# Kernel tuning notes

Measured on AMD Instinct MI355X. Metric: run time of the kernel, lower is better.

Reference implementation:

```python
import jax, jax.numpy as jnp
import numpy as np

N_LAYER, N_HEAD, D_MODEL, D_K, D_HIDDEN = 8, 8, 512, 64, 2048
N_CONTEXT, N_DICT, MAG = 1024, 8192, 0.05
B, T = 8, 1024


def _sinusoidal_pos(n_context, d_model):
    i2 = np.arange(0, d_model, 2)
    inv = 1.0 / (10000.0 ** (i2 / d_model))
    ang = np.arange(n_context, dtype=np.float32)[:, None] * inv[None, :]
    pe = np.zeros((1, n_context, d_model), np.float32)
    pe[0, :, 0::2] = np.sin(ang)
    pe[0, :, 1::2] = np.cos(ang)
    return jnp.asarray(pe)


def setup_inputs() -> dict:
    key = jax.random.key(0)
    ks = jax.random.split(key, 10)
    p = lambda k, *s: jax.random.normal(k, s, jnp.float32) * MAG
    return {
        "x": jax.random.randint(ks[0], (B, T), 0, N_DICT),
        "last_only": False,
        "capture_stats": False,
        "embedding": p(ks[1], N_DICT, D_MODEL),
        "pos_embedding": _sinusoidal_pos(N_CONTEXT, D_MODEL),  # fixedpos='True', not trained
        "wq": p(ks[2], N_LAYER, N_HEAD, D_MODEL, D_K),
        "wk": p(ks[3], N_LAYER, N_HEAD, D_MODEL, D_K),
        "wv": p(ks[4], N_LAYER, N_HEAD, D_MODEL, D_MODEL),
        "mlp0": p(ks[5], N_LAYER, D_MODEL, D_HIDDEN),
        "mlpb": p(ks[6], N_LAYER, 1, D_HIDDEN),
        "mlp1": p(ks[7], N_LAYER, D_HIDDEN, D_MODEL),
        "unembedding": p(ks[8], D_MODEL, N_DICT),
        "bias": p(ks[9], 1, 1, N_DICT),
    }


def _ln(x):
    # torch LayerNorm(elementwise_affine=False, bias=False), eps=1e-5, biased var
    mu = jnp.mean(x, axis=-1, keepdims=True)
    var = jnp.mean((x - mu) ** 2, axis=-1, keepdims=True)
    return (x - mu) * jax.lax.rsqrt(var + 1e-5)


def reference(x, last_only, capture_stats, embedding, pos_embedding,
              wq, wk, wv, mlp0, mlpb, mlp1, unembedding, bias):
    del capture_stats  # stats path disabled (capture_stats=False)
    t = x.shape[1]
    h = embedding[x] + pos_embedding[:, :t, :]   # [B,T,M]
    h = _ln(h)                                    # enorm='True', lmul = 1/ldiv = 1
    mask = jnp.tril(jnp.ones((t, t), dtype=bool))

    def layer(h, params):
        wq_l, wk_l, wv_l, m0, mb, m1 = params
        q = jnp.einsum('btm,hmq->bhtq', h, wq_l)
        k = jnp.einsum('bom,hmk->bhok', h, wk_l)
        v = jnp.einsum('bom,hmv->bhov', h, wv_l)
        attn = jnp.einsum('bhtq,bhoq->bhto', q, k)
        # exp(clamp(.,max=50)) then tril then sum-normalize (NOT softmax)
        attn = jnp.where(mask, jnp.exp(jnp.minimum(attn, 50.0)), 0.0)
        attn = attn / (jnp.sum(attn, axis=-1, keepdims=True) + 1e-10)
        vsum = jnp.einsum('bhto,bhov->btv', attn, v)  # sums over heads
        h = _ln(h + vsum)                              # amul = 1, lmul = 1
        y = jax.nn.relu(jnp.einsum('btm,mh->bth', h, m0) + mb)
        y = jnp.einsum('bth,hm->btm', y, m1)
        h = _ln(h + y)                                 # pmul = 1, lmul = 1
        return h, None

    h, _ = jax.lax.scan(layer, h, (wq, wk, wv, mlp0, mlpb, mlp1))
    if last_only:
        h = h[:, -1:, :]
    return jnp.einsum('btm,md->btd', h, unembedding) + bias
```

## Files before the change

kernel.cpp:

```cpp
#include <hip/hip_runtime.h>
#include <hip/hip_bf16.h>

#define BB 8
#define TT 1024
#define DM 512
#define NH 8
#define DK 64
#define DH 2048
#define NL 8
#define ND 8192

typedef __attribute__((ext_vector_type(8))) short short8v;
typedef __attribute__((ext_vector_type(8))) _Float16 f16x8;
typedef __attribute__((ext_vector_type(4))) float f32x4;
typedef __attribute__((ext_vector_type(4))) unsigned short ushort4v;
typedef unsigned short u16;

#define MFMA16(a, b, c) __builtin_amdgcn_mfma_f32_16x16x32_bf16(a, b, c, 0, 0, 0)
#define MFMAH(a, b, c)  __builtin_amdgcn_mfma_f32_16x16x32_f16(a, b, c, 0, 0, 0)

__device__ __forceinline__ u16 bf16_bits(float f) {
  union { __hip_bfloat16 h; u16 u; } cv;
  cv.h = __float2bfloat16(f);
  return cv.u;
}
__device__ __forceinline__ float bits_to_f32(u16 u) {
  union { __hip_bfloat16 h; u16 u; } cv;
  cv.u = u;
  return __bfloat162float(cv.h);
}

__device__ __forceinline__ void gload16(const void* g, void* l) {
  __builtin_amdgcn_global_load_lds(
      (const __attribute__((address_space(1))) unsigned int*)g,
      (__attribute__((address_space(3))) unsigned int*)l, 16, 0, 0);
}

#define WAITVM(N) asm volatile("s_waitcnt vmcnt(" #N ")" ::: "memory")
#define WAITLGKM() asm volatile("s_waitcnt lgkmcnt(0)" ::: "memory")
#define BAR() { __builtin_amdgcn_s_barrier(); asm volatile("" ::: "memory"); }

__device__ __forceinline__ void block_reduce2(float& a, float& b) {
  #pragma unroll
  for (int off = 32; off > 0; off >>= 1) {
    a += __shfl_down(a, off, 64);
    b += __shfl_down(b, off, 64);
  }
  __shared__ float sa[4], sb[4];
  int w = threadIdx.x >> 6;
  if ((threadIdx.x & 63) == 0) { sa[w] = a; sb[w] = b; }
  __syncthreads();
  if (threadIdx.x == 0) {
    sa[0] = sa[0] + sa[1] + sa[2] + sa[3];
    sb[0] = sb[0] + sb[1] + sb[2] + sb[3];
  }
  __syncthreads();
  a = sa[0]; b = sb[0];
}

__global__ __launch_bounds__(256) void embed_ln_kernel(
    const int* __restrict__ x, const float* __restrict__ emb,
    const float* __restrict__ pos, float* __restrict__ h,
    u16* __restrict__ hh, _Float16* __restrict__ hf) {
  int bt = blockIdx.x;
  int t = bt & (TT - 1);
  int tid = threadIdx.x;
  int row = x[bt];
  float v0 = emb[(size_t)row * DM + tid]       + pos[(size_t)t * DM + tid];
  float v1 = emb[(size_t)row * DM + tid + 256] + pos[(size_t)t * DM + tid + 256];
  float s = v0 + v1, sq = v0 * v0 + v1 * v1;
  block_reduce2(s, sq);
  float mu  = s * (1.0f / DM);
  float var = sq * (1.0f / DM) - mu * mu;
  float rs  = rsqrtf(var + 1e-5f);
  float r0 = (v0 - mu) * rs, r1 = (v1 - mu) * rs;
  h[(size_t)bt * DM + tid] = r0;
  h[(size_t)bt * DM + tid + 256] = r1;
  hh[(size_t)bt * DM + tid] = bf16_bits(r0);
  hh[(size_t)bt * DM + tid + 256] = bf16_bits(r1);
  hf[(size_t)bt * DM + tid] = (_Float16)r0;
  hf[(size_t)bt * DM + tid + 256] = (_Float16)r1;
}

template<bool BF16ADD>
__global__ __launch_bounds__(256) void ln_residual_kernel(
    float* __restrict__ h, const void* __restrict__ add_,
    u16* __restrict__ hh, _Float16* __restrict__ hf) {
  int bt = blockIdx.x;
  int tid = threadIdx.x;
  float v0 = h[(size_t)bt * DM + tid];
  float v1 = h[(size_t)bt * DM + tid + 256];
  if (BF16ADD) {
    const u16* add = (const u16*)add_;
    v0 += bits_to_f32(add[(size_t)bt * DM + tid]);
    v1 += bits_to_f32(add[(size_t)bt * DM + tid + 256]);
  } else {
    const float* add = (const float*)add_;
    v0 += add[(size_t)bt * DM + tid];
    v1 += add[(size_t)bt * DM + tid + 256];
  }
  float s = v0 + v1, sq = v0 * v0 + v1 * v1;
  block_reduce2(s, sq);
  float mu  = s * (1.0f / DM);
  float var = sq * (1.0f / DM) - mu * mu;
  float rs  = rsqrtf(var + 1e-5f);
  float r0 = (v0 - mu) * rs, r1 = (v1 - mu) * rs;
  h[(size_t)bt * DM + tid] = r0;
  h[(size_t)bt * DM + tid + 256] = r1;
  hh[(size_t)bt * DM + tid] = bf16_bits(r0);
  hh[(size_t)bt * DM + tid + 256] = bf16_bits(r1);
  hf[(size_t)bt * DM + tid] = (_Float16)r0;
  hf[(size_t)bt * DM + tid + 256] = (_Float16)r1;
}

__global__ __launch_bounds__(256) void transpose_hT(
    const float* __restrict__ h, u16* __restrict__ hT) {
  __shared__ float T[64][65];
  int t0 = blockIdx.x * 64;
  int d0 = blockIdx.y * 64;
  int tid = threadIdx.x;
  #pragma unroll
  for (int rep = 0; rep < 16; ++rep) {
    int idx = rep * 256 + tid;
    int i = idx >> 6, j = idx & 63;
    T[i][j] = h[(size_t)(t0 + i) * DM + d0 + j];
  }
  __syncthreads();
  #pragma unroll
  for (int rep = 0; rep < 16; ++rep) {
    int idx = rep * 256 + tid;
    int j = idx >> 6, i = idx & 63;
    hT[(size_t)(d0 + j) * (BB * TT) + t0 + i] = bf16_bits(T[i][j]);
  }
}

__global__ __launch_bounds__(256) void transpose_layer(
    const float* __restrict__ wq, const float* __restrict__ wk,
    const float* __restrict__ wv, const float* __restrict__ w0,
    const float* __restrict__ w1,
    _Float16* __restrict__ qkT, u16* __restrict__ vT2,
    u16* __restrict__ t0o, u16* __restrict__ t1o) {
  __shared__ float T[64][65];
  int t = blockIdx.x;
  const float* in;
  _Float16* of = nullptr;
  u16* ob = nullptr;
  int K, Nb;
  bool vmode = false;
  if (t < 64)       { in = wq; of = qkT;          K = 512;  Nb = 64; }
  else if (t < 128) { in = wk; of = qkT + 262144; K = 512;  Nb = 64;   t -= 64; }
  else if (t < 640) { in = wv; ob = vT2;          K = 512;  Nb = 512;  t -= 128; vmode = true; }
  else if (t < 896) { in = w0; ob = t0o;          K = 512;  Nb = 2048; t -= 640; }
  else              { in = w1; ob = t1o;          K = 2048; Nb = 512;  t -= 896; }
  int ntx = K >> 6;
  int k0 = (t % ntx) * 64, n0 = (t / ntx) * 64;
  int g = n0 / Nb;
  const float* src = in + (size_t)g * K * Nb + (n0 - g * Nb);
  int tid = threadIdx.x;
  #pragma unroll
  for (int rep = 0; rep < 16; ++rep) {
    int idx = rep * 256 + tid;
    int i = idx >> 6, j = idx & 63;
    T[i][j] = src[(size_t)(k0 + i) * Nb + j];
  }
  __syncthreads();
  #pragma unroll
  for (int rep = 0; rep < 16; ++rep) {
    int idx = rep * 256 + tid;
    int j = idx >> 6, i = idx & 63;
    float v = T[i][j];
    if (vmode) {
      vT2[(size_t)(n0 - g * Nb + j) * (NH * DM) + g * Nb + k0 + i] = bf16_bits(v);
    } else if (of) {
      of[(size_t)(n0 + j) * K + k0 + i] = (_Float16)v;
    } else {
      ob[(size_t)(n0 + j) * K + k0 + i] = bf16_bits(v);
    }
  }
}

__global__ __launch_bounds__(256) void transpose_ue(
    const float* __restrict__ ue, u16* __restrict__ ueT) {
  __shared__ float T[64][65];
  int tid = threadIdx.x;
  int k0 = blockIdx.x * 64, n0 = blockIdx.y * 64;
  #pragma unroll
  for (int rep = 0; rep < 16; ++rep) {
    int idx = rep * 256 + tid;
    int i = idx >> 6, j = idx & 63;
    T[i][j] = ue[(size_t)(k0 + i) * ND + n0 + j];
  }
  __syncthreads();
  #pragma unroll
  for (int rep = 0; rep < 16; ++rep) {
    int idx = rep * 256 + tid;
    int j = idx >> 6, i = idx & 63;
    ueT[(size_t)(n0 + j) * DM + k0 + i] = bf16_bits(T[i][j]);
  }
}

template<int MODE>
__global__ __launch_bounds__(256, 2) void gemm_mfma(
    const u16* __restrict__ A, const u16* __restrict__ Bt,
    const float* __restrict__ bias, void* __restrict__ Oo,
    int M, int N, int K) {
  __shared__ u16 As[2][8192];
  __shared__ u16 Bs[2][8192];
  int tid = threadIdx.x;
  int lane = tid & 63, w = tid >> 6;
  int l15 = lane & 15, g = lane >> 4;
  int m0 = blockIdx.x * 128, n0 = blockIdx.y * 128;
  int wr = w >> 1, wc = w & 1;
  int nt = K >> 6;

  f32x4 acc[4][4];
  #pragma unroll
  for (int i = 0; i < 4; ++i)
    #pragma unroll
    for (int j = 0; j < 4; ++j)
      #pragma unroll
      for (int r = 0; r < 4; ++r) acc[i][j][r] = 0.f;

  auto stage = [&](int t, int buf) {
    int k0 = t << 6;
    #pragma unroll
    for (int j = 0; j < 4; ++j) {
      int idx = j * 256 + tid;
      int row = idx >> 3, cs = (idx & 7) ^ (row & 7);
      gload16(A + (size_t)(m0 + row) * K + k0 + cs * 8, &As[buf][idx * 8]);
    }
    #pragma unroll
    for (int j = 0; j < 4; ++j) {
      int idx = j * 256 + tid;
      int row = idx >> 3, cs = (idx & 7) ^ (row & 7);
      gload16(Bt + (size_t)(n0 + row) * K + k0 + cs * 8, &Bs[buf][idx * 8]);
    }
  };

  stage(0, 0);
  for (int t = 0; t < nt; ++t) {
    int cur = t & 1;
    if (t + 1 < nt) {
      stage(t + 1, cur ^ 1);
      WAITVM(8);
    } else {
      WAITVM(0);
    }
    BAR();
    short8v af[4][2], bf[4][2];
    #pragma unroll
    for (int mi = 0; mi < 4; ++mi) {
      int row = wr * 64 + mi * 16 + l15;
      #pragma unroll
      for (int ks = 0; ks < 2; ++ks) {
        int ch = (ks * 4 + g) ^ (row & 7);
        af[mi][ks] = *(const short8v*)&As[cur][row * 64 + ch * 8];
      }
    }
    #pragma unroll
    for (int ni = 0; ni < 4; ++ni) {
      int row = wc * 64 + ni * 16 + l15;
      #pragma unroll
      for (int ks = 0; ks < 2; ++ks) {
        int ch = (ks * 4 + g) ^ (row & 7);
        bf[ni][ks] = *(const short8v*)&Bs[cur][row * 64 + ch * 8];
      }
    }
    __builtin_amdgcn_s_setprio(1);
    #pragma unroll
    for (int mi = 0; mi < 4; ++mi)
      #pragma unroll
      for (int ni = 0; ni < 4; ++ni) {
        acc[mi][ni] = MFMA16(af[mi][0], bf[ni][0], acc[mi][ni]);
        acc[mi][ni] = MFMA16(af[mi][1], bf[ni][1], acc[mi][ni]);
      }
    __builtin_amdgcn_s_setprio(0);
    BAR();
  }

  #pragma unroll
  for (int mi = 0; mi < 4; ++mi) {
    #pragma unroll
    for (int ni = 0; ni < 4; ++ni) {
      int mrow = m0 + wr * 64 + mi * 16 + g * 4;
      int ncol = n0 + wc * 64 + ni * 16 + l15;
      if (MODE == 1) {
        float bv = bias[ncol];
        #pragma unroll
        for (int r = 0; r < 4; ++r)
          ((u16*)Oo)[(size_t)(mrow + r) * N + ncol] =
              bf16_bits(fmaxf(acc[mi][ni][r] + bv, 0.f));
      } else if (MODE == 2) {
        #pragma unroll
        for (int r = 0; r < 4; ++r)
          ((float*)Oo)[(size_t)(mrow + r) * N + ncol] = acc[mi][ni][r];
      } else if (MODE == 3) {
        float bv = bias[ncol];
        #pragma unroll
        for (int r = 0; r < 4; ++r)
          ((float*)Oo)[(size_t)(mrow + r) * N + ncol] = acc[mi][ni][r] + bv;
      } else {
        #pragma unroll
        for (int r = 0; r < 4; ++r)
          ((u16*)Oo)[(size_t)(mrow + r) * N + ncol] = bf16_bits(acc[mi][ni][r]);
      }
    }
  }
}

template<int MODE>
__global__ __launch_bounds__(256, 2) void gemm_n64(
    const u16* __restrict__ A, const u16* __restrict__ Bt,
    void* __restrict__ Oo, int M, int N, int K) {
  __shared__ u16 As[2][8192];
  __shared__ u16 Bs[2][4096];
  int tid = threadIdx.x;
  int lane = tid & 63, w = tid >> 6;
  int l15 = lane & 15, g = lane >> 4;
  int m0 = blockIdx.x * 128, n0 = blockIdx.y * 64;
  int wr = w >> 1, wc = w & 1;
  int nt = K >> 6;

  f32x4 acc[4][2];
  #pragma unroll
  for (int i = 0; i < 4; ++i)
    #pragma unroll
    for (int j = 0; j < 2; ++j)
      #pragma unroll
      for (int r = 0; r < 4; ++r) acc[i][j][r] = 0.f;

  auto stage = [&](int t, int buf) {
    int k0 = t << 6;
    #pragma unroll
    for (int j = 0; j < 4; ++j) {
      int idx = j * 256 + tid;
      int row = idx >> 3, cs = (idx & 7) ^ (row & 7);
      gload16(A + (size_t)(m0 + row) * K + k0 + cs * 8, &As[buf][idx * 8]);
    }
    #pragma unroll
    for (int j = 0; j < 2; ++j) {
      int idx = j * 256 + tid;
      int row = idx >> 3, cs = (idx & 7) ^ (row & 7);
      gload16(Bt + (size_t)(n0 + row) * K + k0 + cs * 8, &Bs[buf][idx * 8]);
    }
  };

  stage(0, 0);
  for (int t = 0; t < nt; ++t) {
    int cur = t & 1;
    if (t + 1 < nt) {
      stage(t + 1, cur ^ 1);
      WAITVM(6);
    } else {
      WAITVM(0);
    }
    BAR();
    short8v af[4][2], bf[2][2];
    #pragma unroll
    for (int mi = 0; mi < 4; ++mi) {
      int row = wr * 64 + mi * 16 + l15;
      #pragma unroll
      for (int ks = 0; ks < 2; ++ks) {
        int ch = (ks * 4 + g) ^ (row & 7);
        af[mi][ks] = *(const short8v*)&As[cur][row * 64 + ch * 8];
      }
    }
    #pragma unroll
    for (int ni = 0; ni < 2; ++ni) {
      int row = wc * 32 + ni * 16 + l15;
      #pragma unroll
      for (int ks = 0; ks < 2; ++ks) {
        int ch = (ks * 4 + g) ^ (row & 7);
        bf[ni][ks] = *(const short8v*)&Bs[cur][row * 64 + ch * 8];
      }
    }
    __builtin_amdgcn_s_setprio(1);
    #pragma unroll
    for (int mi = 0; mi < 4; ++mi)
      #pragma unroll
      for (int ni = 0; ni < 2; ++ni) {
        acc[mi][ni] = MFMA16(af[mi][0], bf[ni][0], acc[mi][ni]);
        acc[mi][ni] = MFMA16(af[mi][1], bf[ni][1], acc[mi][ni]);
      }
    __builtin_amdgcn_s_setprio(0);
    BAR();
  }

  #pragma unroll
  for (int mi = 0; mi < 4; ++mi) {
    #pragma unroll
    for (int ni = 0; ni < 2; ++ni) {
      int mrow = m0 + wr * 64 + mi * 16 + g * 4;
      int ncol = n0 + wc * 32 + ni * 16 + l15;
      if (MODE == 2) {
        #pragma unroll
        for (int r = 0; r < 4; ++r)
          ((float*)Oo)[(size_t)(mrow + r) * N + ncol] = acc[mi][ni][r];
      } else {
        #pragma unroll
        for (int r = 0; r < 4; ++r)
          ((u16*)Oo)[(size_t)(mrow + r) * N + ncol] = bf16_bits(acc[mi][ni][r]);
      }
    }
  }
}

__global__ __launch_bounds__(256, 2) void gemm_qk_f16(
    const _Float16* __restrict__ A, const _Float16* __restrict__ Bt,
    _Float16* __restrict__ Oq, int K) {
  __shared__ _Float16 As[2][8192];
  __shared__ _Float16 Bs[2][8192];
  int tid = threadIdx.x;
  int lane = tid & 63, w = tid >> 6;
  int l15 = lane & 15, g = lane >> 4;
  int m0 = blockIdx.x * 128, n0 = blockIdx.y * 128;
  int wr = w >> 1, wc = w & 1;
  int nt = K >> 6;

  f32x4 acc[4][4];
  #pragma unroll
  for (int i = 0; i < 4; ++i)
    #pragma unroll
    for (int j = 0; j < 4; ++j)
      #pragma unroll
      for (int r = 0; r < 4; ++r) acc[i][j][r] = 0.f;

  auto stage = [&](int t, int buf) {
    int k0 = t << 6;
    #pragma unroll
    for (int j = 0; j < 4; ++j) {
      int idx = j * 256 + tid;
      int row = idx >> 3, cs = (idx & 7) ^ (row & 7);
      gload16(A + (size_t)(m0 + row) * K + k0 + cs * 8, &As[buf][idx * 8]);
    }
    #pragma unroll
    for (int j = 0; j < 4; ++j) {
      int idx = j * 256 + tid;
      int row = idx >> 3, cs = (idx & 7) ^ (row & 7);
      gload16(Bt + (size_t)(n0 + row) * K + k0 + cs * 8, &Bs[buf][idx * 8]);
    }
  };

  stage(0, 0);
  for (int t = 0; t < nt; ++t) {
    int cur = t & 1;
    if (t + 1 < nt) {
      stage(t + 1, cur ^ 1);
      WAITVM(8);
    } else {
      WAITVM(0);
    }
    BAR();
    f16x8 af[4][2], bf[4][2];
    #pragma unroll
    for (int mi = 0; mi < 4; ++mi) {
      int row = wr * 64 + mi * 16 + l15;
      #pragma unroll
      for (int ks = 0; ks < 2; ++ks) {
        int ch = (ks * 4 + g) ^ (row & 7);
        af[mi][ks] = *(const f16x8*)&As[cur][row * 64 + ch * 8];
      }
    }
    #pragma unroll
    for (int ni = 0; ni < 4; ++ni) {
      int row = wc * 64 + ni * 16 + l15;
      #pragma unroll
      for (int ks = 0; ks < 2; ++ks) {
        int ch = (ks * 4 + g) ^ (row & 7);
        bf[ni][ks] = *(const f16x8*)&Bs[cur][row * 64 + ch * 8];
      }
    }
    __builtin_amdgcn_s_setprio(1);
    #pragma unroll
    for (int mi = 0; mi < 4; ++mi)
      #pragma unroll
      for (int ni = 0; ni < 4; ++ni) {
        acc[mi][ni] = MFMAH(af[mi][0], bf[ni][0], acc[mi][ni]);
        acc[mi][ni] = MFMAH(af[mi][1], bf[ni][1], acc[mi][ni]);
      }
    __builtin_amdgcn_s_setprio(0);
    BAR();
  }

  #pragma unroll
  for (int mi = 0; mi < 4; ++mi) {
    #pragma unroll
    for (int ni = 0; ni < 4; ++ni) {
      int mrow = m0 + wr * 64 + mi * 16 + g * 4;
      int ncol = n0 + wc * 64 + ni * 16 + l15;
      _Float16* dst = Oq;
      int nc = ncol;
      if (nc >= 512) { dst = Oq + 4194304; nc -= 512; }
      int head = nc >> 6, dk = nc & (DK - 1);
      int bb = mrow >> 10;
      #pragma unroll
      for (int r = 0; r < 4; ++r) {
        int t = (mrow + r) & (TT - 1);
        dst[(((size_t)bb * NH + head) * TT + t) * DK + dk] = (_Float16)acc[mi][ni][r];
      }
    }
  }
}

__global__ __launch_bounds__(256, 2) void attn_mfma_kernel(
    const _Float16* __restrict__ qp, const _Float16* __restrict__ kp,
    const u16* __restrict__ hT, u16* __restrict__ o) {
  __shared__ __align__(16) u16 Pl[2][64 * 64];
  __shared__ __align__(16) _Float16 Kl[2][64 * 64];
  __shared__ float rs_lds[64];

  int tid = threadIdx.x;
  int lane = tid & 63;
  int w = tid >> 6;
  int l15 = lane & 15, g = lane >> 4;
  int blk = blockIdx.x;
  int bh = blk & 63;
  int tt = 15 - (blk >> 6);
  int b = bh >> 3;

  if (tid < 64) rs_lds[tid] = 0.f;

  auto stageK = [&](int ot, int buf) {
    int ob = ot * 64;
    #pragma unroll
    for (int j = 0; j < 2; ++j) {
      int idx = j * 256 + tid;
      int row = idx >> 3, cs = (idx & 7) ^ (row & 7);
      gload16(kp + ((size_t)bh * TT + ob + row) * DK + cs * 8, &Kl[buf][idx * 8]);
    }
  };

  size_t qbase = (((size_t)bh * TT) + tt * 64 + w * 16 + l15) * DK + g * 8;
  f16x8 qf[2];
  qf[0] = *(const f16x8*)(qp + qbase);
  qf[1] = *(const f16x8*)(qp + qbase + 32);

  f32x4 oacc[4][8];
  #pragma unroll
  for (int qt = 0; qt < 4; ++qt)
    #pragma unroll
    for (int dv = 0; dv < 8; ++dv)
      #pragma unroll
      for (int r = 0; r < 4; ++r) oacc[qt][dv][r] = 0.f;

  stageK(0, 0);
  WAITVM(0);
  __syncthreads();

  for (int ot = 0; ot <= tt; ++ot) {
    int ob = ot * 64;
    bool diag = (ot == tt);
    int buf = ot & 1;
    if (ot < tt) stageK(ot + 1, buf ^ 1);
    f32x4 sacc[4];
    #pragma unroll
    for (int ct = 0; ct < 4; ++ct)
      #pragma unroll
      for (int r = 0; r < 4; ++r) sacc[ct][r] = 0.f;
    __builtin_amdgcn_s_setprio(1);
    #pragma unroll
    for (int ct = 0; ct < 4; ++ct) {
      int row = ct * 16 + l15;
      f16x8 k0 = *(const f16x8*)&Kl[buf][row * 64 + ((g) ^ (row & 7)) * 8];
      f16x8 k1 = *(const f16x8*)&Kl[buf][row * 64 + ((4 + g) ^ (row & 7)) * 8];
      sacc[ct] = MFMAH(qf[0], k0, sacc[ct]);
      sacc[ct] = MFMAH(qf[1], k1, sacc[ct]);
    }
    __builtin_amdgcn_s_setprio(0);
    size_t vbase = ((size_t)(w * 128 + l15)) * (BB * TT) + b * TT + ob + g * 8;
    short8v vf0[8];
    #pragma unroll
    for (int dv = 0; dv < 8; ++dv)
      vf0[dv] = *(const short8v*)(hT + vbase + (size_t)dv * 16 * (BB * TT));
    float psum[4] = {0.f, 0.f, 0.f, 0.f};
    #pragma unroll
    for (int ct = 0; ct < 4; ++ct) {
      #pragma unroll
      for (int r = 0; r < 4; ++r) {
        float s = sacc[ct][r];
        float p = __expf(fminf(s, 50.f));
        if (diag && (ct * 16 + l15 > w * 16 + g * 4 + r)) p = 0.f;
        psum[r] += p;
        int q = w * 16 + g * 4 + r;
        int byte = (q * 128 + (ct * 16 + l15) * 2) ^ ((q & 7) << 4);
        *(u16*)((char*)Pl[buf] + byte) = bf16_bits(p);
      }
    }
    #pragma unroll
    for (int r = 0; r < 4; ++r) {
      float v = psum[r];
      v += __shfl_xor(v, 1, 16);
      v += __shfl_xor(v, 2, 16);
      v += __shfl_xor(v, 4, 16);
      v += __shfl_xor(v, 8, 16);
      if (l15 == 0) rs_lds[w * 16 + g * 4 + r] += v;
    }
    WAITVM(8);
    WAITLGKM();
    BAR();
    short8v vf1[8];
    #pragma unroll
    for (int dv = 0; dv < 8; ++dv)
      vf1[dv] = *(const short8v*)(hT + vbase + 32 + (size_t)dv * 16 * (BB * TT));
    short8v pf[4];
    #pragma unroll
    for (int qt = 0; qt < 4; ++qt) {
      int q = qt * 16 + l15;
      int byte = (q * 128 + g * 16) ^ ((q & 7) << 4);
      pf[qt] = *(short8v*)((char*)Pl[buf] + byte);
    }
    __builtin_amdgcn_s_setprio(1);
    #pragma unroll
    for (int dv = 0; dv < 8; ++dv)
      #pragma unroll
      for (int qt = 0; qt < 4; ++qt)
        oacc[qt][dv] = MFMA16(pf[qt], vf0[dv], oacc[qt][dv]);
    __builtin_amdgcn_s_setprio(0);
    #pragma unroll
    for (int qt = 0; qt < 4; ++qt) {
      int q = qt * 16 + l15;
      int byte = (q * 128 + 64 + g * 16) ^ ((q & 7) << 4);
      pf[qt] = *(short8v*)((char*)Pl[buf] + byte);
    }
    __builtin_amdgcn_s_setprio(1);
    #pragma unroll
    for (int dv = 0; dv < 8; ++dv)
      #pragma unroll
      for (int qt = 0; qt < 4; ++qt)
        oacc[qt][dv] = MFMA16(pf[qt], vf1[dv], oacc[qt][dv]);
    __builtin_amdgcn_s_setprio(0);
  }
  __syncthreads();
  int hh2 = bh & 7;
  #pragma unroll
  for (int qt = 0; qt < 4; ++qt) {
    #pragma unroll
    for (int r = 0; r < 4; ++r) {
      int q = qt * 16 + g * 4 + r;
      float rs = 1.0f / (rs_lds[q] + 1e-10f);
      size_t rowbase = ((size_t)(b * TT + tt * 64 + q)) * (NH * DM) + hh2 * DM + w * 128 + l15;
      #pragma unroll
      for (int dv = 0; dv < 8; ++dv)
        o[rowbase + dv * 16] = bf16_bits(oacc[qt][dv][r] * rs);
    }
  }
}

extern "C" void kernel_launch(void* const* d_in, const int* in_sizes, int n_in,
                              void* d_out, int out_size, void* d_ws, size_t ws_size,
                              hipStream_t stream) {
  (void)in_sizes; (void)n_in; (void)out_size; (void)ws_size;
  const int*   x   = (const int*)d_in[0];
  const float* emb = (const float*)d_in[3];
  const float* pos = (const float*)d_in[4];
  const float* wq  = (const float*)d_in[5];
  const float* wk  = (const float*)d_in[6];
  const float* wv  = (const float*)d_in[7];
  const float* m0  = (const float*)d_in[8];
  const float* mb  = (const float*)d_in[9];
  const float* m1  = (const float*)d_in[10];
  const float* ue  = (const float*)d_in[11];
  const float* ub  = (const float*)d_in[12];
  float* out = (float*)d_out;
  float* ws  = (float*)d_ws;

  const int M = BB * TT;

  float*    h    = ws;
  u16*      hh   = (u16*)(ws + 4194304);
  _Float16* hf16 = (_Float16*)(ws + 6291456);
  float*    yb   = ws + 8388608;
  u16*      ueT  = (u16*)(ws + 12582912);

  u16* outus = (u16*)d_out;
  u16* hT   = outus;
  u16* hid  = outus + 4194304;
  u16* vsum = outus + 20971520;
  _Float16* qf16 = (_Float16*)(outus + 33554432);
  u16* wT = outus + 41943040;
  _Float16* wqkT = (_Float16*)wT;
  u16* wvT2 = wT + 524288;
  u16* w0T  = wT + 2621440;
  u16* w1T  = wT + 3670016;
  u16* Ob   = outus + 67108864;

  embed_ln_kernel<<<M, 256, 0, stream>>>(x, emb, pos, h, hh, hf16);
  transpose_hT<<<dim3(128, 8), 256, 0, stream>>>(h, hT);

  for (int l = 0; l < NL; ++l) {
    transpose_layer<<<1152, 256, 0, stream>>>(
        wq + (size_t)l * NH * DM * DK, wk + (size_t)l * NH * DM * DK,
        wv + (size_t)l * NH * DM * DM, m0 + (size_t)l * DM * DH,
        m1 + (size_t)l * DH * DM,
        wqkT, wvT2, w0T, w1T);
    gemm_qk_f16<<<dim3(64, 8), 256, 0, stream>>>(hf16, wqkT, qf16, DM);
    attn_mfma_kernel<<<BB * NH * (TT / 64), 256, 0, stream>>>(
        qf16, qf16 + 4194304, hT, Ob);
    gemm_n64<4><<<dim3(64, 8), 256, 0, stream>>>(Ob, wvT2, vsum, M, DM, NH * DM);
    ln_residual_kernel<true><<<M, 256, 0, stream>>>(h, vsum, hh, hf16);
    gemm_mfma<1><<<dim3(64, 16), 256, 0, stream>>>(hh, w0T, mb + (size_t)l * DH, hid, M, DH, DM);
    gemm_n64<2><<<dim3(64, 8), 256, 0, stream>>>(hid, w1T, yb, M, DM, DH);
    ln_residual_kernel<false><<<M, 256, 0, stream>>>(h, yb, hh, hf16);
    if (l + 1 < NL)
      transpose_hT<<<dim3(128, 8), 256, 0, stream>>>(h, hT);
  }
  transpose_ue<<<dim3(8, 128), 256, 0, stream>>>(ue, ueT);
  gemm_mfma<3><<<dim3(64, 64), 256, 0, stream>>>(hh, ueT, ub, out, M, ND, DM);
}
```

Before: 2.204 ms.

## Split-K skinny GEMMs, batch all weight transposes up front, fuse partial-sum LN

The two N=512 GEMMs (attention value projection and MLP down-projection) now split K in two along a grid z dimension, which doubles the block count from 512 to 1024 to fill the CUs better. Each half writes an fp32 partial buffer, and the residual-LayerNorm kernel sums both partials. All per-layer weight transposes plus the unembedding transpose run in one large launch before the layer loop, into buffers for each layer inside the output scratch. This removes eight serialized launches from the critical path. In exchange there is extra fp32 partial traffic, and the residual add for the value projection now reads fp32 instead of bf16.

```diff
diff --git a/kernel.cpp b/kernel.cpp
--- a/kernel.cpp
+++ b/kernel.cpp
@@ -39,6 +39,10 @@
 #define WAITVM(N) asm volatile("s_waitcnt vmcnt(" #N ")" ::: "memory")
 #define WAITLGKM() asm volatile("s_waitcnt lgkmcnt(0)" ::: "memory")
 #define BAR() { __builtin_amdgcn_s_barrier(); asm volatile("" ::: "memory"); }
+
+#define WL_SZ 4718592
+#define WR0  41943040
+#define WR1 100663296
 
 __device__ __forceinline__ void block_reduce2(float& a, float& b) {
   #pragma unroll
@@ -82,35 +86,28 @@
   hf[(size_t)bt * DM + tid + 256] = (_Float16)r1;
 }
 
-template<bool BF16ADD>
-__global__ __launch_bounds__(256) void ln_residual_kernel(
-    float* __restrict__ h, const void* __restrict__ add_,
+__global__ __launch_bounds__(256) void ln2_residual_kernel(
+    float* __restrict__ h, const float* __restrict__ p0,
+    const float* __restrict__ p1,
     u16* __restrict__ hh, _Float16* __restrict__ hf) {
   int bt = blockIdx.x;
   int tid = threadIdx.x;
-  float v0 = h[(size_t)bt * DM + tid];
-  float v1 = h[(size_t)bt * DM + tid + 256];
-  if (BF16ADD) {
-    const u16* add = (const u16*)add_;
-    v0 += bits_to_f32(add[(size_t)bt * DM + tid]);
-    v1 += bits_to_f32(add[(size_t)bt * DM + tid + 256]);
-  } else {
-    const float* add = (const float*)add_;
-    v0 += add[(size_t)bt * DM + tid];
-    v1 += add[(size_t)bt * DM + tid + 256];
-  }
+  size_t i0 = (size_t)bt * DM + tid;
+  size_t i1 = i0 + 256;
+  float v0 = h[i0] + p0[i0] + p1[i0];
+  float v1 = h[i1] + p0[i1] + p1[i1];
   float s = v0 + v1, sq = v0 * v0 + v1 * v1;
   block_reduce2(s, sq);
   float mu  = s * (1.0f / DM);
   float var = sq * (1.0f / DM) - mu * mu;
   float rs  = rsqrtf(var + 1e-5f);
   float r0 = (v0 - mu) * rs, r1 = (v1 - mu) * rs;
-  h[(size_t)bt * DM + tid] = r0;
-  h[(size_t)bt * DM + tid + 256] = r1;
-  hh[(size_t)bt * DM + tid] = bf16_bits(r0);
-  hh[(size_t)bt * DM + tid + 256] = bf16_bits(r1);
-  hf[(size_t)bt * DM + tid] = (_Float16)r0;
-  hf[(size_t)bt * DM + tid + 256] = (_Float16)r1;
+  h[i0] = r0;
+  h[i1] = r1;
+  hh[i0] = bf16_bits(r0);
+  hh[i1] = bf16_bits(r1);
+  hf[i0] = (_Float16)r0;
+  hf[i1] = (_Float16)r1;
 }
 
 __global__ __launch_bounds__(256) void transpose_hT(
@@ -134,29 +131,54 @@
   }
 }
 
-__global__ __launch_bounds__(256) void transpose_layer(
+__global__ __launch_bounds__(256) void prep_weights(
     const float* __restrict__ wq, const float* __restrict__ wk,
-    const float* __restrict__ wv, const float* __restrict__ w0,
-    const float* __restrict__ w1,
-    _Float16* __restrict__ qkT, u16* __restrict__ vT2,
-    u16* __restrict__ t0o, u16* __restrict__ t1o) {
+    const float* __restrict__ wv, const float* __restrict__ m0,
+    const float* __restrict__ m1, const float* __restrict__ ue,
+    u16* __restrict__ outus, u16* __restrict__ ueT) {
   __shared__ float T[64][65];
-  int t = blockIdx.x;
+  int bx = blockIdx.x;
+  int tid = threadIdx.x;
+  if (bx >= 9216) {
+    int t = bx - 9216;
+    int k0 = (t & 7) * 64, n0 = (t >> 3) * 64;
+    #pragma unroll
+    for (int rep = 0; rep < 16; ++rep) {
+      int idx = rep * 256 + tid;
+      int i = idx >> 6, j = idx & 63;
+      T[i][j] = ue[(size_t)(k0 + i) * ND + n0 + j];
+    }
+    __syncthreads();
+    #pragma unroll
+    for (int rep = 0; rep < 16; ++rep) {
+      int idx = rep * 256 + tid;
+      int j = idx >> 6, i = idx & 63;
+      ueT[(size_t)(n0 + j) * DM + k0 + i] = bf16_bits(T[i][j]);
+    }
+    return;
+  }
+  int l = bx / 1152;
+  int t = bx % 1152;
+  u16* base = (l < 5) ? outus + WR0 + (size_t)l * WL_SZ
+                      : outus + WR1 + (size_t)(l - 5) * WL_SZ;
+  _Float16* qkT = (_Float16*)base;
+  u16* vT2 = base + 524288;
+  u16* t0o = base + 2621440;
+  u16* t1o = base + 3670016;
   const float* in;
   _Float16* of = nullptr;
   u16* ob = nullptr;
   int K, Nb;
   bool vmode = false;
-  if (t < 64)       { in = wq; of = qkT;          K = 512;  Nb = 64; }
-  else if (t < 128) { in = wk; of = qkT + 262144; K = 512;  Nb = 64;   t -= 64; }
-  else if (t < 640) { in = wv; ob = vT2;          K = 512;  Nb = 512;  t -= 128; vmode = true; }
-  else if (t < 896) { in = w0; ob = t0o;          K = 512;  Nb = 2048; t -= 640; }
-  else              { in = w1; ob = t1o;          K = 2048; Nb = 512;  t -= 896; }
+  if (t < 64)       { in = wq + (size_t)l * NH * DM * DK; of = qkT;          K = 512;  Nb = 64; }
+  else if (t < 128) { in = wk + (size_t)l * NH * DM * DK; of = qkT + 262144; K = 512;  Nb = 64;   t -= 64; }
+  else if (t < 640) { in = wv + (size_t)l * NH * DM * DM; ob = vT2;          K = 512;  Nb = 512;  t -= 128; vmode = true; }
+  else if (t < 896) { in = m0 + (size_t)l * DM * DH;      ob = t0o;          K = 512;  Nb = 2048; t -= 640; }
+  else              { in = m1 + (size_t)l * DH * DM;      ob = t1o;          K = 2048; Nb = 512;  t -= 896; }
   int ntx = K >> 6;
   int k0 = (t % ntx) * 64, n0 = (t / ntx) * 64;
   int g = n0 / Nb;
   const float* src = in + (size_t)g * K * Nb + (n0 - g * Nb);
-  int tid = threadIdx.x;
   #pragma unroll
   for (int rep = 0; rep < 16; ++rep) {
     int idx = rep * 256 + tid;
@@ -179,26 +201,6 @@
   }
 }
 
-__global__ __launch_bounds__(256) void transpose_ue(
-    const float* __restrict__ ue, u16* __restrict__ ueT) {
-  __shared__ float T[64][65];
-  int tid = threadIdx.x;
-  int k0 = blockIdx.x * 64, n0 = blockIdx.y * 64;
-  #pragma unroll
-  for (int rep = 0; rep < 16; ++rep) {
-    int idx = rep * 256 + tid;
-    int i = idx >> 6, j = idx & 63;
-    T[i][j] = ue[(size_t)(k0 + i) * ND + n0 + j];
-  }
-  __syncthreads();
-  #pragma unroll
-  for (int rep = 0; rep < 16; ++rep) {
-    int idx = rep * 256 + tid;
-    int j = idx >> 6, i = idx & 63;
-    ueT[(size_t)(n0 + j) * DM + k0 + i] = bf16_bits(T[i][j]);
-  }
-}
-
 template<int MODE>
 __global__ __launch_bounds__(256, 2) void gemm_mfma(
     const u16* __restrict__ A, const u16* __restrict__ Bt,
@@ -290,36 +292,30 @@
         for (int r = 0; r < 4; ++r)
           ((u16*)Oo)[(size_t)(mrow + r) * N + ncol] =
               bf16_bits(fmaxf(acc[mi][ni][r] + bv, 0.f));
-      } else if (MODE == 2) {
-        #pragma unroll
-        for (int r = 0; r < 4; ++r)
-          ((float*)Oo)[(size_t)(mrow + r) * N + ncol] = acc[mi][ni][r];
-      } else if (MODE == 3) {
+      } else {
         float bv = bias[ncol];
         #pragma unroll
         for (int r = 0; r < 4; ++r)
           ((float*)Oo)[(size_t)(mrow + r) * N + ncol] = acc[mi][ni][r] + bv;
-      } else {
-        #pragma unroll
-        for (int r = 0; r < 4; ++r)
-          ((u16*)Oo)[(size_t)(mrow + r) * N + ncol] = bf16_bits(acc[mi][ni][r]);
-      }
-    }
-  }
-}
-
-template<int MODE>
-__global__ __launch_bounds__(256, 2) void gemm_n64(
+      }
+    }
+  }
+}
+
+__global__ __launch_bounds__(256, 2) void gemm_skinny(
     const u16* __restrict__ A, const u16* __restrict__ Bt,
-    void* __restrict__ Oo, int M, int N, int K) {
+    float* __restrict__ Oo, int M, int N, int K) {
   __shared__ u16 As[2][8192];
   __shared__ u16 Bs[2][4096];
   int tid = threadIdx.x;
   int lane = tid & 63, w = tid >> 6;
   int l15 = lane & 15, g = lane >> 4;
   int m0 = blockIdx.x * 128, n0 = blockIdx.y * 64;
+  int kz = blockIdx.z;
+  int KH = K >> 1;
+  int kbase = kz * KH;
   int wr = w >> 1, wc = w & 1;
-  int nt = K >> 6;
+  int nt = KH >> 6;
 
   f32x4 acc[4][2];
   #pragma unroll
@@ -330,7 +326,7 @@
       for (int r = 0; r < 4; ++r) acc[i][j][r] = 0.f;
 
   auto stage = [&](int t, int buf) {
-    int k0 = t << 6;
+    int k0 = kbase + (t << 6);
     #pragma unroll
     for (int j = 0; j < 4; ++j) {
       int idx = j * 256 + tid;
@@ -386,21 +382,16 @@
     BAR();
   }
 
+  float* Op = Oo + (size_t)kz * M * N;
   #pragma unroll
   for (int mi = 0; mi < 4; ++mi) {
     #pragma unroll
     for (int ni = 0; ni < 2; ++ni) {
       int mrow = m0 + wr * 64 + mi * 16 + g * 4;
       int ncol = n0 + wc * 32 + ni * 16 + l15;
-      if (MODE == 2) {
-        #pragma unroll
-        for (int r = 0; r < 4; ++r)
-          ((float*)Oo)[(size_t)(mrow + r) * N + ncol] = acc[mi][ni][r];
-      } else {
-        #pragma unroll
-        for (int r = 0; r < 4; ++r)
-          ((u16*)Oo)[(size_t)(mrow + r) * N + ncol] = bf16_bits(acc[mi][ni][r]);
-      }
+      #pragma unroll
+      for (int r = 0; r < 4; ++r)
+        Op[(size_t)(mrow + r) * N + ncol] = acc[mi][ni][r];
     }
   }
 }
@@ -669,41 +660,38 @@
   float*    h    = ws;
   u16*      hh   = (u16*)(ws + 4194304);
   _Float16* hf16 = (_Float16*)(ws + 6291456);
-  float*    yb   = ws + 8388608;
-  u16*      ueT  = (u16*)(ws + 12582912);
+  u16*      ueT  = (u16*)(ws + 8388608);
 
   u16* outus = (u16*)d_out;
   u16* hT   = outus;
+  float* vpart = (float*)(outus + 4194304);
   u16* hid  = outus + 4194304;
-  u16* vsum = outus + 20971520;
   _Float16* qf16 = (_Float16*)(outus + 33554432);
-  u16* wT = outus + 41943040;
-  _Float16* wqkT = (_Float16*)wT;
-  u16* wvT2 = wT + 524288;
-  u16* w0T  = wT + 2621440;
-  u16* w1T  = wT + 3670016;
   u16* Ob   = outus + 67108864;
-
+  float* ypart = (float*)Ob;
+
+  prep_weights<<<10240, 256, 0, stream>>>(wq, wk, wv, m0, m1, ue, outus, ueT);
   embed_ln_kernel<<<M, 256, 0, stream>>>(x, emb, pos, h, hh, hf16);
   transpose_hT<<<dim3(128, 8), 256, 0, stream>>>(h, hT);
 
   for (int l = 0; l < NL; ++l) {
-    transpose_layer<<<1152, 256, 0, stream>>>(
-        wq + (size_t)l * NH * DM * DK, wk + (size_t)l * NH * DM * DK,
-        wv + (size_t)l * NH * DM * DM, m0 + (size_t)l * DM * DH,
-        m1 + (size_t)l * DH * DM,
-        wqkT, wvT2, w0T, w1T);
+    u16* wb = (l < 5) ? outus + WR0 + (size_t)l * WL_SZ
+                      : outus + WR1 + (size_t)(l - 5) * WL_SZ;
+    _Float16* wqkT = (_Float16*)wb;
+    u16* wvT2 = wb + 524288;
+    u16* w0T  = wb + 2621440;
+    u16* w1T  = wb + 3670016;
+
     gemm_qk_f16<<<dim3(64, 8), 256, 0, stream>>>(hf16, wqkT, qf16, DM);
     attn_mfma_kernel<<<BB * NH * (TT / 64), 256, 0, stream>>>(
         qf16, qf16 + 4194304, hT, Ob);
-    gemm_n64<4><<<dim3(64, 8), 256, 0, stream>>>(Ob, wvT2, vsum, M, DM, NH * DM);
-    ln_residual_kernel<true><<<M, 256, 0, stream>>>(h, vsum, hh, hf16);
+    gemm_skinny<<<dim3(64, 8, 2), 256, 0, stream>>>(Ob, wvT2, vpart, M, DM, NH * DM);
+    ln2_residual_kernel<<<M, 256, 0, stream>>>(h, vpart, vpart + 4194304, hh, hf16);
     gemm_mfma<1><<<dim3(64, 16), 256, 0, stream>>>(hh, w0T, mb + (size_t)l * DH, hid, M, DH, DM);
-    gemm_n64<2><<<dim3(64, 8), 256, 0, stream>>>(hid, w1T, yb, M, DM, DH);
-    ln_residual_kernel<false><<<M, 256, 0, stream>>>(h, yb, hh, hf16);
+    gemm_skinny<<<dim3(64, 8, 2), 256, 0, stream>>>(hid, w1T, ypart, M, DM, DH);
+    ln2_residual_kernel<<<M, 256, 0, stream>>>(h, ypart, ypart + 4194304, hh, hf16);
     if (l + 1 < NL)
       transpose_hT<<<dim3(128, 8), 256, 0, stream>>>(h, hT);
   }
-  transpose_ue<<<dim3(8, 128), 256, 0, stream>>>(ue, ueT);
   gemm_mfma<3><<<dim3(64, 64), 256, 0, stream>>>(hh, ueT, ub, out, M, ND, DM);
 }
```

New measurement: 2.473 ms. 1.12x slower.
